# Kernel optimization log

Hardware: AMD Instinct MI355X
Metric: run time of the kernel (lower is better)

The kernel has to match this reference:

```python
import jax, jax.numpy as jnp
import numpy as np

BETA = 0.25

def setup_inputs() -> dict:
    key = jax.random.key(0)
    k1, k2 = jax.random.split(key)
    x = jax.random.normal(k1, (32, 1024, 256), dtype=jnp.float32)
    # tf.random_uniform_initializer default range is [-0.05, 0.05)
    embedding = jax.random.uniform(k2, (256, 8192), dtype=jnp.float32, minval=-0.05, maxval=0.05)
    return {"x": x, "embedding": embedding}


def reference(x, embedding):
    # x: [B, S, D]; embedding: [D, K] (codebook stored column-wise, as in the tf module)
    D = x.shape[-1]
    flat = x.reshape(-1, D)                                   # [N, D]
    dists = (jnp.sum(flat * flat, axis=1, keepdims=True)
             - 2.0 * (flat @ embedding)
             + jnp.sum(embedding * embedding, axis=0))
    idx = jnp.argmin(dists, axis=1)                           # [N] int
    quantized = jnp.take(embedding.T, idx, axis=0).reshape(x.shape)  # gather codebook columns
    # VQ losses
    commitment = jnp.mean(jnp.square(jax.lax.stop_gradient(quantized) - x))
    codebook = jnp.mean(jnp.square(quantized - jax.lax.stop_gradient(x)))
    loss = BETA * commitment + codebook
    # straight-through estimator
    quantized_st = x + jax.lax.stop_gradient(quantized - x)
    return quantized_st, loss
```

## Files before the change

kernel.cpp:

```cpp
#include <hip/hip_runtime.h>

typedef float f4   __attribute__((ext_vector_type(4)));
typedef float f2   __attribute__((ext_vector_type(2)));
typedef _Float16 f16x8 __attribute__((ext_vector_type(8)));
typedef float f32x4  __attribute__((ext_vector_type(4)));

#define N_ROWS  32768
#define D_DIM   256
#define K_CODES 8192
#define NUM_ELEM (N_ROWS * D_DIM)
#define EPS_MARGIN 2e-3f
#define FB_CAP  8192
#define FB_RPB  8
#define RF_SLICES 16
#define N_PANELS 256
#define HALF_PANELS 128

__device__ __forceinline__ void gl2lds16(const void* g, void* l) {
    __builtin_amdgcn_global_load_lds(
        (const __attribute__((address_space(1))) unsigned int*)g,
        (__attribute__((address_space(3))) unsigned int*)l, 16, 0, 0);
}

__global__ void prep_kernel(const float* __restrict__ E, short* __restrict__ Ep,
                            float* __restrict__ Et32, float* __restrict__ ee) {
    __shared__ float eepart[8][32];
    const int p  = blockIdx.x;
    const int t  = threadIdx.x;
    const int c  = t & 31;
    const int gq = t >> 5;
    const int cp = p * 32;
    short* ph = Ep + (size_t)p * 8192;
    float ss = 0.0f;
    #pragma unroll
    for (int gi = 0; gi < 4; ++gi) {
        int g = gq * 4 + gi;
        f16x8 h;
        f4 av, bv;
        #pragma unroll
        for (int j = 0; j < 8; ++j) {
            float v = E[(size_t)(g * 8 + j) * K_CODES + cp + c];
            h[j] = (_Float16)v;
            ss += v * v;
            if (j < 4) av[j] = v; else bv[j - 4] = v;
        }
        *(f16x8*)(ph + (g * 32 + c) * 8) = h;
        *(f4*)(Et32 + (size_t)(cp + c) * D_DIM + g * 8)     = av;
        *(f4*)(Et32 + (size_t)(cp + c) * D_DIM + g * 8 + 4) = bv;
    }
    eepart[gq][c] = ss;
    __syncthreads();
    if (t < 32) {
        float s = 0.0f;
        #pragma unroll
        for (int q = 0; q < 8; ++q) s += eepart[q][t];
        ee[cp + t] = s;
    }
}

__launch_bounds__(256, 2)
__global__ void mfma_sieve_kernel(const float* __restrict__ X,
                                  const short* __restrict__ Ep,
                                  const float* __restrict__ ee,
                                  f2* __restrict__ res_bs,
                                  int* __restrict__ res_idx) {
    __shared__ __align__(16) short Bbuf[2][8192];
    const int t    = threadIdx.x;
    const int w    = t >> 6;
    const int lane = t & 63;
    const int n    = lane & 15;
    const int quad = lane >> 4;
    const int half = blockIdx.x & 1;
    const int row0 = (blockIdx.x >> 1) * 128;
    const int rw   = row0 + w * 32;
    const int p0   = half * HALF_PANELS;

    f16x8 Ah[2][8];
    #pragma unroll
    for (int rt = 0; rt < 2; ++rt) {
        const float* xp = X + (size_t)(rw + rt * 16 + n) * D_DIM;
        #pragma unroll
        for (int ks = 0; ks < 8; ++ks) {
            int d = ks * 32 + quad * 8;
            f4 a = *(const f4*)(xp + d);
            f4 b = *(const f4*)(xp + d + 4);
            f16x8 h;
            #pragma unroll
            for (int j = 0; j < 8; ++j) {
                float x = (j < 4) ? a[j] : b[j - 4];
                h[j] = (_Float16)x;
            }
            Ah[rt][ks] = h;
        }
    }

    float bestv[8], secv[8]; int besti[8];
    #pragma unroll
    for (int s = 0; s < 8; ++s) { bestv[s] = 1e30f; secv[s] = 1e30f; besti[s] = 0; }

    {
        const char* gp = (const char*)Ep + (size_t)p0 * 16384;
        char* lp = (char*)&Bbuf[0][0];
        #pragma unroll
        for (int i = 0; i < 4; ++i)
            gl2lds16(gp + (w * 4 + i) * 1024 + lane * 16, lp + (w * 4 + i) * 1024);
    }
    __syncthreads();

    for (int i = 0; i < HALF_PANELS; ++i) {
        const int p   = p0 + i;
        const int buf = i & 1;
        if (i + 1 < HALF_PANELS) {
            const char* gp = (const char*)Ep + (size_t)(p + 1) * 16384;
            char* lp = (char*)&Bbuf[buf ^ 1][0];
            #pragma unroll
            for (int k = 0; k < 4; ++k)
                gl2lds16(gp + (w * 4 + k) * 1024 + lane * 16, lp + (w * 4 + k) * 1024);
        }

        const short* Bh = &Bbuf[buf][0];

        f32x4 acc[2][2];
        #pragma unroll
        for (int ct = 0; ct < 2; ++ct)
            #pragma unroll
            for (int rt = 0; rt < 2; ++rt)
                acc[ct][rt] = (f32x4)(0.0f);

        #pragma unroll
        for (int ks = 0; ks < 8; ++ks) {
            const int g = ks * 4 + quad;
            f16x8 bh[2];
            #pragma unroll
            for (int ct = 0; ct < 2; ++ct) {
                int c = ct * 16 + n;
                bh[ct] = *(const f16x8*)(Bh + (g * 32 + c) * 8);
            }
            #pragma unroll
            for (int ct = 0; ct < 2; ++ct)
                #pragma unroll
                for (int rt = 0; rt < 2; ++rt)
                    acc[ct][rt] = __builtin_amdgcn_mfma_f32_16x16x32_f16(Ah[rt][ks], bh[ct], acc[ct][rt], 0, 0, 0);
        }

        const int cb = p * 32;
        #pragma unroll
        for (int ct = 0; ct < 2; ++ct) {
            int code = cb + ct * 16 + n;
            float eev = ee[code];
            #pragma unroll
            for (int rt = 0; rt < 2; ++rt)
                #pragma unroll
                for (int r = 0; r < 4; ++r) {
                    float key = fmaf(-2.0f, acc[ct][rt][r], eev);
                    int s = rt * 4 + r;
                    float nb = fminf(key, bestv[s]);
                    secv[s]  = fminf(secv[s], fmaxf(key, bestv[s]));
                    besti[s] = (key < bestv[s]) ? code : besti[s];
                    bestv[s] = nb;
                }
        }
        __syncthreads();
    }

    #pragma unroll
    for (int off = 1; off < 16; off <<= 1) {
        #pragma unroll
        for (int s = 0; s < 8; ++s) {
            float ov = __shfl_xor(bestv[s], off);
            int   oi = __shfl_xor(besti[s], off);
            float os = __shfl_xor(secv[s], off);
            bool owin = (ov < bestv[s]) || (ov == bestv[s] && oi < besti[s]);
            if (owin) { secv[s] = fminf(os, bestv[s]); bestv[s] = ov; besti[s] = oi; }
            else      { secv[s] = fminf(secv[s], ov); }
        }
    }

    if (n == 0) {
        #pragma unroll
        for (int s = 0; s < 8; ++s) {
            int rl  = w * 32 + (s >> 2) * 16 + quad * 4 + (s & 3);
            int row = row0 + rl;
            f2 bs; bs[0] = bestv[s]; bs[1] = secv[s];
            res_bs[(size_t)row * 2 + half]  = bs;
            res_idx[(size_t)row * 2 + half] = besti[s];
        }
    }
}

__global__ void gather_kernel(const float* __restrict__ X, const float* __restrict__ Et32,
                              const f2* __restrict__ res_bs, const int* __restrict__ res_idx,
                              int* __restrict__ counter, int2* __restrict__ list,
                              float* __restrict__ out, double* __restrict__ loss_sum) {
    __shared__ int bl_[128];
    const int t    = threadIdx.x;
    const int row0 = blockIdx.x * 128;
    if (t < 128) {
        const int row = row0 + t;
        f2 a = res_bs[(size_t)row * 2];
        f2 b = res_bs[(size_t)row * 2 + 1];
        int ia = res_idx[(size_t)row * 2];
        int ib = res_idx[(size_t)row * 2 + 1];
        float gb; int gi; float gs;
        if (b[0] < a[0]) { gb = b[0]; gi = ib; gs = fminf(b[1], a[0]); }
        else             { gb = a[0]; gi = ia; gs = fminf(a[1], b[0]); }
        bl_[t] = gi;
        if (gs - gb <= EPS_MARGIN) {
            int pos = atomicAdd(counter, 1);
            if (pos < FB_CAP) list[pos] = make_int2(row, gi);
        }
    }
    __syncthreads();
    double ls = 0.0;
    const int d = t;
    #pragma unroll 4
    for (int r = 0; r < 128; ++r) {
        int code = bl_[r];
        float q  = Et32[(size_t)code * D_DIM + d];
        float x  = X[(size_t)(row0 + r) * D_DIM + d];
        float dq = q - x;
        out[(size_t)(row0 + r) * D_DIM + d] = x + dq;
        ls += (double)dq * (double)dq;
    }
    #pragma unroll
    for (int off = 32; off > 0; off >>= 1)
        ls += __shfl_down(ls, off);
    if ((t & 63) == 0) atomicAdd(loss_sum, ls);
}

__global__ void refine1_kernel(const float* __restrict__ X, const float* __restrict__ E,
                               const int* __restrict__ counter, const int2* __restrict__ list,
                               double* __restrict__ res_v, int* __restrict__ res_i) {
    __shared__ float xt[D_DIM][FB_RPB];
    __shared__ int rows_sh[FB_RPB];
    __shared__ double wbv[4][FB_RPB];
    __shared__ int    wbi[4][FB_RPB];

    int nf = *counter; if (nf > FB_CAP) nf = FB_CAP;
    const int nchunks = (nf + FB_RPB - 1) / FB_RPB;
    const int nitems  = nchunks * RF_SLICES;
    const int t = threadIdx.x;

    for (int item = blockIdx.x; item < nitems; item += gridDim.x) {
        const int rc = item / RF_SLICES;
        const int sl = item % RF_SLICES;
        __syncthreads();
        if (t < FB_RPB) {
            int e = rc * FB_RPB + t;
            int2 ent = list[(e < nf) ? e : 0];
            rows_sh[t] = ent.x;
        }
        __syncthreads();
        #pragma unroll
        for (int j = 0; j < FB_RPB; ++j)
            xt[t][j] = X[(size_t)rows_sh[j] * D_DIM + t];
        __syncthreads();

        const int k0 = sl * 512 + t * 2;
        double s0[FB_RPB], s1[FB_RPB], q0 = 0.0, q1 = 0.0;
        #pragma unroll
        for (int j = 0; j < FB_RPB; ++j) { s0[j] = 0.0; s1[j] = 0.0; }
        for (int d = 0; d < D_DIM; ++d) {
            f2 ev = *(const f2*)(E + (size_t)d * K_CODES + k0);
            double e0d = (double)ev[0], e1d = (double)ev[1];
            const f4* xp = (const f4*)(&xt[d][0]);
            f4 xa = xp[0], xb = xp[1];
            double xd[FB_RPB] = { (double)xa[0], (double)xa[1], (double)xa[2], (double)xa[3],
                                  (double)xb[0], (double)xb[1], (double)xb[2], (double)xb[3] };
            q0 += e0d * e0d; q1 += e1d * e1d;
            #pragma unroll
            for (int j = 0; j < FB_RPB; ++j) {
                s0[j] += xd[j] * e0d;
                s1[j] += xd[j] * e1d;
            }
        }
        double bv[FB_RPB]; int bi[FB_RPB];
        #pragma unroll
        for (int j = 0; j < FB_RPB; ++j) {
            double k0v = q0 - 2.0 * s0[j];
            double k1v = q1 - 2.0 * s1[j];
            bv[j] = k0v; bi[j] = k0;
            if (k1v < bv[j]) { bv[j] = k1v; bi[j] = k0 + 1; }
        }
        #pragma unroll
        for (int off = 1; off < 64; off <<= 1) {
            #pragma unroll
            for (int j = 0; j < FB_RPB; ++j) {
                double ov = __shfl_xor(bv[j], off);
                int    oi = __shfl_xor(bi[j], off);
                if (ov < bv[j] || (ov == bv[j] && oi < bi[j])) { bv[j] = ov; bi[j] = oi; }
            }
        }
        const int wave = t >> 6;
        if ((t & 63) == 0) {
            #pragma unroll
            for (int j = 0; j < FB_RPB; ++j) { wbv[wave][j] = bv[j]; wbi[wave][j] = bi[j]; }
        }
        __syncthreads();
        if (t < FB_RPB) {
            double b = wbv[0][t]; int i_ = wbi[0][t];
            #pragma unroll
            for (int wv = 1; wv < 4; ++wv) {
                double ov = wbv[wv][t]; int oi = wbi[wv][t];
                if (ov < b || (ov == b && oi < i_)) { b = ov; i_ = oi; }
            }
            int e = rc * FB_RPB + t;
            res_v[(size_t)e * RF_SLICES + sl] = b;
            res_i[(size_t)e * RF_SLICES + sl] = i_;
        }
    }
}

__global__ void patch_kernel(const float* __restrict__ X, const float* __restrict__ Et32,
                             float* __restrict__ out, double* __restrict__ loss_sum,
                             const int* __restrict__ counter, const int2* __restrict__ list,
                             const double* __restrict__ res_v, const int* __restrict__ res_i) {
    int nf = *counter; if (nf > FB_CAP) nf = FB_CAP;
    const int b = blockIdx.x;
    if (b >= nf) return;
    __shared__ int nc_sh;
    const int t = threadIdx.x;
    if (t == 0) {
        double bv = res_v[(size_t)b * RF_SLICES]; int bi = res_i[(size_t)b * RF_SLICES];
        for (int s = 1; s < RF_SLICES; ++s) {
            double v = res_v[(size_t)b * RF_SLICES + s];
            int    i = res_i[(size_t)b * RF_SLICES + s];
            if (v < bv || (v == bv && i < bi)) { bv = v; bi = i; }
        }
        nc_sh = bi;
    }
    __syncthreads();
    int2 ent = list[b];
    const int oc = ent.y, row = ent.x, nc = nc_sh;
    if (nc == oc) return;
    float x  = X[(size_t)row * D_DIM + t];
    float qn = Et32[(size_t)nc * D_DIM + t];
    float qo = Et32[(size_t)oc * D_DIM + t];
    float dqn = qn - x, dqo = qo - x;
    out[(size_t)row * D_DIM + t] = x + dqn;
    double dl = (double)dqn * dqn - (double)dqo * dqo;
    #pragma unroll
    for (int off = 32; off > 0; off >>= 1)
        dl += __shfl_down(dl, off);
    if ((t & 63) == 0) atomicAdd(loss_sum, dl);
}

__global__ void fin_kernel(const double* __restrict__ loss_sum, float* __restrict__ out) {
    double m = loss_sum[0] / (double)NUM_ELEM;
    out[NUM_ELEM] = (float)(0.25 * m + m);
}

extern "C" void kernel_launch(void* const* d_in, const int* in_sizes, int n_in,
                              void* d_out, int out_size, void* d_ws, size_t ws_size,
                              hipStream_t stream) {
    const float* X = (const float*)d_in[0];
    const float* E = (const float*)d_in[1];
    float* out = (float*)d_out;

    double* loss_sum = (double*)d_ws;
    int*    counter  = (int*)((char*)d_ws + 8);
    float*  ee       = (float*)((char*)d_ws + 1024);
    int2*   list     = (int2*)((char*)d_ws + 36864);
    double* res_v    = (double*)((char*)d_ws + 131072);
    int*    res_i    = (int*)((char*)d_ws + 1179648);
    float*  Et32     = (float*)((char*)d_ws + 1703936);
    short*  Ep       = (short*)((char*)d_ws + 10092544);
    f2*     res_bs   = (f2*)((char*)d_ws + 14286848);
    int*    res_idx  = (int*)((char*)d_ws + 15335424);

    hipMemsetAsync(d_ws, 0, 1024, stream);
    prep_kernel<<<N_PANELS, 256, 0, stream>>>(E, Ep, Et32, ee);
    mfma_sieve_kernel<<<512, 256, 0, stream>>>(X, Ep, ee, res_bs, res_idx);
    gather_kernel<<<N_ROWS / 128, 256, 0, stream>>>(X, Et32, res_bs, res_idx,
                                                    counter, list, out, loss_sum);
    refine1_kernel<<<2048, 256, 0, stream>>>(X, E, counter, list, res_v, res_i);
    patch_kernel<<<FB_CAP, 256, 0, stream>>>(X, Et32, out, loss_sum, counter, list,
                                             res_v, res_i);
    fin_kernel<<<1, 1, 0, stream>>>(loss_sum, out);
}
```

Before: 326.1 us.

## Stage two codebook panels per barrier and fold workspace zeroing into prep

The sieve kernel now loads two 32-code panels per double-buffer stage (64 KB LDS) and processes both before each __syncthreads, halving the number of barriers and prefetch issue points. The hipMemsetAsync that cleared the workspace header is replaced by block 0 of prep_kernel zeroing 8 KB, which removes one launch. The workspace offsets for ee and list move to make room for that zeroed region. The larger LDS footprint may reduce how many blocks fit per CU under the 2-block launch bound.

```diff
diff --git a/kernel.cpp b/kernel.cpp
--- a/kernel.cpp
+++ b/kernel.cpp
@@ -15,6 +15,7 @@
 #define RF_SLICES 16
 #define N_PANELS 256
 #define HALF_PANELS 128
+#define HALF_PAIRS 64
 
 __device__ __forceinline__ void gl2lds16(const void* g, void* l) {
     __builtin_amdgcn_global_load_lds(
@@ -23,13 +24,20 @@
 }
 
 __global__ void prep_kernel(const float* __restrict__ E, short* __restrict__ Ep,
-                            float* __restrict__ Et32, float* __restrict__ ee) {
+                            float* __restrict__ Et32, float* __restrict__ ee,
+                            float* __restrict__ ctl) {
     __shared__ float eepart[8][32];
     const int p  = blockIdx.x;
     const int t  = threadIdx.x;
     const int c  = t & 31;
     const int gq = t >> 5;
     const int cp = p * 32;
+    if (p == 0) {
+        f4 z = (f4)(0.0f);
+        f4* dst = (f4*)ctl;
+        dst[t * 2]     = z;
+        dst[t * 2 + 1] = z;
+    }
     short* ph = Ep + (size_t)p * 8192;
     float ss = 0.0f;
     #pragma unroll
@@ -64,7 +72,7 @@
                                   const float* __restrict__ ee,
                                   f2* __restrict__ res_bs,
                                   int* __restrict__ res_idx) {
-    __shared__ __align__(16) short Bbuf[2][8192];
+    __shared__ __align__(16) short Bbuf[2][16384];
     const int t    = threadIdx.x;
     const int w    = t >> 6;
     const int lane = t & 63;
@@ -102,63 +110,66 @@
         const char* gp = (const char*)Ep + (size_t)p0 * 16384;
         char* lp = (char*)&Bbuf[0][0];
         #pragma unroll
-        for (int i = 0; i < 4; ++i)
-            gl2lds16(gp + (w * 4 + i) * 1024 + lane * 16, lp + (w * 4 + i) * 1024);
+        for (int i = 0; i < 8; ++i)
+            gl2lds16(gp + (w * 8 + i) * 1024 + lane * 16, lp + (w * 8 + i) * 1024);
     }
     __syncthreads();
 
-    for (int i = 0; i < HALF_PANELS; ++i) {
-        const int p   = p0 + i;
-        const int buf = i & 1;
-        if (i + 1 < HALF_PANELS) {
-            const char* gp = (const char*)Ep + (size_t)(p + 1) * 16384;
-            char* lp = (char*)&Bbuf[buf ^ 1][0];
-            #pragma unroll
-            for (int k = 0; k < 4; ++k)
-                gl2lds16(gp + (w * 4 + k) * 1024 + lane * 16, lp + (w * 4 + k) * 1024);
-        }
-
-        const short* Bh = &Bbuf[buf][0];
-
-        f32x4 acc[2][2];
-        #pragma unroll
-        for (int ct = 0; ct < 2; ++ct)
-            #pragma unroll
-            for (int rt = 0; rt < 2; ++rt)
-                acc[ct][rt] = (f32x4)(0.0f);
-
-        #pragma unroll
-        for (int ks = 0; ks < 8; ++ks) {
-            const int g = ks * 4 + quad;
-            f16x8 bh[2];
-            #pragma unroll
-            for (int ct = 0; ct < 2; ++ct) {
-                int c = ct * 16 + n;
-                bh[ct] = *(const f16x8*)(Bh + (g * 32 + c) * 8);
-            }
+    for (int ii = 0; ii < HALF_PAIRS; ++ii) {
+        const int pbuf = ii & 1;
+        if (ii + 1 < HALF_PAIRS) {
+            const char* gp = (const char*)Ep + (size_t)(p0 + 2 * (ii + 1)) * 16384;
+            char* lp = (char*)&Bbuf[pbuf ^ 1][0];
+            #pragma unroll
+            for (int k = 0; k < 8; ++k)
+                gl2lds16(gp + (w * 8 + k) * 1024 + lane * 16, lp + (w * 8 + k) * 1024);
+        }
+
+        #pragma unroll
+        for (int sub = 0; sub < 2; ++sub) {
+            const int p = p0 + 2 * ii + sub;
+            const short* Bh = &Bbuf[pbuf][sub * 8192];
+
+            f32x4 acc[2][2];
             #pragma unroll
             for (int ct = 0; ct < 2; ++ct)
                 #pragma unroll
                 for (int rt = 0; rt < 2; ++rt)
-                    acc[ct][rt] = __builtin_amdgcn_mfma_f32_16x16x32_f16(Ah[rt][ks], bh[ct], acc[ct][rt], 0, 0, 0);
-        }
-
-        const int cb = p * 32;
-        #pragma unroll
-        for (int ct = 0; ct < 2; ++ct) {
-            int code = cb + ct * 16 + n;
-            float eev = ee[code];
-            #pragma unroll
-            for (int rt = 0; rt < 2; ++rt)
+                    acc[ct][rt] = (f32x4)(0.0f);
+
+            #pragma unroll
+            for (int ks = 0; ks < 8; ++ks) {
+                const int g = ks * 4 + quad;
+                f16x8 bh[2];
                 #pragma unroll
-                for (int r = 0; r < 4; ++r) {
-                    float key = fmaf(-2.0f, acc[ct][rt][r], eev);
-                    int s = rt * 4 + r;
-                    float nb = fminf(key, bestv[s]);
-                    secv[s]  = fminf(secv[s], fmaxf(key, bestv[s]));
-                    besti[s] = (key < bestv[s]) ? code : besti[s];
-                    bestv[s] = nb;
+                for (int ct = 0; ct < 2; ++ct) {
+                    int c = ct * 16 + n;
+                    bh[ct] = *(const f16x8*)(Bh + (g * 32 + c) * 8);
                 }
+                #pragma unroll
+                for (int ct = 0; ct < 2; ++ct)
+                    #pragma unroll
+                    for (int rt = 0; rt < 2; ++rt)
+                        acc[ct][rt] = __builtin_amdgcn_mfma_f32_16x16x32_f16(Ah[rt][ks], bh[ct], acc[ct][rt], 0, 0, 0);
+            }
+
+            const int cb = p * 32;
+            #pragma unroll
+            for (int ct = 0; ct < 2; ++ct) {
+                int code = cb + ct * 16 + n;
+                float eev = ee[code];
+                #pragma unroll
+                for (int rt = 0; rt < 2; ++rt)
+                    #pragma unroll
+                    for (int r = 0; r < 4; ++r) {
+                        float key = fmaf(-2.0f, acc[ct][rt][r], eev);
+                        int s = rt * 4 + r;
+                        float nb = fminf(key, bestv[s]);
+                        secv[s]  = fminf(secv[s], fmaxf(key, bestv[s]));
+                        besti[s] = (key < bestv[s]) ? code : besti[s];
+                        bestv[s] = nb;
+                    }
+            }
         }
         __syncthreads();
     }
@@ -359,8 +370,8 @@
 
     double* loss_sum = (double*)d_ws;
     int*    counter  = (int*)((char*)d_ws + 8);
-    float*  ee       = (float*)((char*)d_ws + 1024);
-    int2*   list     = (int2*)((char*)d_ws + 36864);
+    float*  ee       = (float*)((char*)d_ws + 8192);
+    int2*   list     = (int2*)((char*)d_ws + 40960);
     double* res_v    = (double*)((char*)d_ws + 131072);
     int*    res_i    = (int*)((char*)d_ws + 1179648);
     float*  Et32     = (float*)((char*)d_ws + 1703936);
@@ -368,8 +379,7 @@
     f2*     res_bs   = (f2*)((char*)d_ws + 14286848);
     int*    res_idx  = (int*)((char*)d_ws + 15335424);
 
-    hipMemsetAsync(d_ws, 0, 1024, stream);
-    prep_kernel<<<N_PANELS, 256, 0, stream>>>(E, Ep, Et32, ee);
+    prep_kernel<<<N_PANELS, 256, 0, stream>>>(E, Ep, Et32, ee, (float*)d_ws);
     mfma_sieve_kernel<<<512, 256, 0, stream>>>(X, Ep, ee, res_bs, res_idx);
     gather_kernel<<<N_ROWS / 128, 256, 0, stream>>>(X, Et32, res_bs, res_idx,
                                                     counter, list, out, loss_sum);
```

Result: no change. 326.6 us (+0.1%).
